# Kernel tuning notes

Hardware: AMD Instinct MI355X
Metric: run time of the kernel (lower is better)

The kernel has to match this reference:

```python
import jax, jax.numpy as jnp
import numpy as np
from jax import lax

V = 100000   # vocab
D = 300      # embedding / input_dim
H = 512      # hidden_dim per direction
T = 8192     # sequence length (batch_size hardcoded to 1 in the module)
TAG = 12     # len(tag_dict)
START = 10
STOP = 11
NEG = -10000.0


def setup_inputs() -> dict:
    key = jax.random.key(0)
    ks = jax.random.split(key, 11)
    s = 1.0 / np.sqrt(H)
    u = lambda k, shp: jax.random.uniform(k, shp, minval=-s, maxval=s)
    transition = jax.random.normal(ks[9], (TAG, TAG))
    transition = transition.at[:, START].set(NEG).at[STOP, :].set(NEG)
    return {
        "sent": jax.random.randint(ks[0], (T,), 0, V, dtype=jnp.int32),
        "emb": jax.random.normal(ks[1], (V, D)) * 0.1,
        "W_ih_f": u(ks[2], (4 * H, D)),
        "W_hh_f": u(ks[3], (4 * H, H)),
        "b_f": u(ks[4], (4 * H,)),
        "W_ih_b": u(ks[5], (4 * H, D)),
        "W_hh_b": u(ks[6], (4 * H, H)),
        "b_b": u(ks[7], (4 * H,)),
        "W_proj": u(ks[8], (TAG, 2 * H)),
        "b_proj": jnp.zeros((TAG,)),
        "transition": transition,
    }


def _lstm_dir(xs, Wih, Whh, b):
    # one-direction LSTM over [T, D] (batch=1 squeezed); torch gate order i,f,g,o
    def step(carry, x):
        h, c = carry
        g = x @ Wih.T + h @ Whh.T + b
        i, f, gg, o = jnp.split(g, 4)
        c = jax.nn.sigmoid(f) * c + jax.nn.sigmoid(i) * jnp.tanh(gg)
        h = jax.nn.sigmoid(o) * jnp.tanh(c)
        return (h, c), h
    z = jnp.zeros((H,), xs.dtype)
    _, hs = lax.scan(step, (z, z), xs)
    return hs


def reference(sent, emb, W_ih_f, W_hh_f, b_f, W_ih_b, W_hh_b, b_b, W_proj, b_proj, transition):
    x = emb[sent]  # [T, D]
    hf = _lstm_dir(x, W_ih_f, W_hh_f, b_f)                 # [T, H]
    hb = _lstm_dir(x[::-1], W_ih_b, W_hh_b, b_b)[::-1]     # [T, H]
    hh = jnp.concatenate([hf, hb], axis=-1)                # [T, 2H]
    feats = jax.nn.log_softmax(hh @ W_proj.T + b_proj, axis=-1)  # [T, TAG]

    # Viterbi decode (self.decode): max over previous tag + transition + emission
    def vstep(v, feat):
        tmp = v[:, None] + transition   # [TAG_prev, TAG_next]
        return tmp.max(axis=0) + feat, jnp.argmax(tmp, axis=0)
    v0 = jnp.full((TAG,), NEG).at[START].set(0.0)
    vT, ptrs = lax.scan(vstep, v0, feats)
    vT = vT + transition[:, STOP]
    score = vT.max()
    best = jnp.argmax(vT)

    # backtrace: best_tags[t] = ptrs[t][best_tags[t+1]], return best_tags[1:T] + [best]
    def back(tag, ptr):
        prev = ptr[tag]
        return prev, prev
    _, ys = lax.scan(back, best, ptrs, reverse=True)  # ys[t] = best_tags[t], t=0..T-1
    tags = jnp.concatenate([ys[1:], best[None]])
    return score, tags
```

## Files before the change

### kernel.cpp

```cpp
#include <hip/hip_runtime.h>
#include <stdint.h>

#define T_LEN 8192
#define HID 512
#define NTAG 12
#define START_TAG 10
#define STOP_TAG 11
#define NEGV -10000.0f

#define H_OFF     0u
#define FEATS_OFF 33554432u
#define CNT_OFF   33947648u

__device__ __forceinline__ float blo(uint32_t u) {
    union { uint32_t i; float f; } x; x.i = u << 16; return x.f;
}
__device__ __forceinline__ float bhi(uint32_t u) {
    union { uint32_t i; float f; } x; x.i = u & 0xffff0000u; return x.f;
}
__device__ __forceinline__ float b2f(uint16_t u) {
    union { uint32_t i; float f; } x; x.i = ((uint32_t)u) << 16; return x.f;
}
__device__ __forceinline__ uint32_t rne16(float f) {
    union { float f; uint32_t i; } x; x.f = f;
    uint32_t u = x.i + 0x7FFFu + ((x.i >> 16) & 1u);
    return u >> 16;
}
__device__ __forceinline__ uint32_t pk(float f0, float f1) {
    return rne16(f0) | (rne16(f1) << 16);
}
__device__ __forceinline__ float sigm(float x) { return 1.0f / (1.0f + expf(-x)); }

__global__ __launch_bounds__(256) void k_probe(
    const uint32_t* __restrict__ embw, const int* __restrict__ sent32, int* __restrict__ cnt)
{
    __shared__ int s_bf16, s_zero;
    const int tid = threadIdx.x;
    if (tid == 0) { s_bf16 = 0; s_zero = 0; }
    __syncthreads();
    uint32_t u = embw[tid * 97 + 5];
    float lo = b2f((uint16_t)(u & 0xFFFFu));
    float hi = b2f((uint16_t)(u >> 16));
    if (fabsf(lo) <= 8.0f && fabsf(hi) <= 8.0f) atomicAdd(&s_bf16, 1);
    if (sent32[2 * tid + 1] == 0) atomicAdd(&s_zero, 1);
    __syncthreads();
    if (tid == 0) {
        cnt[32] = (s_bf16 < 224) ? 1 : 0;
        cnt[33] = (s_zero >= 250) ? 1 : 0;
    }
    if (tid < 32) cnt[tid] = 0;
}

__global__ __launch_bounds__(512) void k_scan(
    const int* __restrict__ sent, const void* __restrict__ emb,
    const void* __restrict__ wih_f, const void* __restrict__ whh_f,
    const void* __restrict__ b_f,
    const void* __restrict__ wih_b, const void* __restrict__ whh_b,
    const void* __restrict__ b_b,
    float* __restrict__ harr, int* __restrict__ cnt)
{
    __shared__ uint16_t wlds[128 * 520];
    __shared__ float hbuf[512];
    __shared__ float partial[4][128];
    __shared__ float gbuf[128];
    __shared__ float xbuf[2][304];

    const int tid = threadIdx.x;
    const int dir = blockIdx.x >> 4;
    const int w   = blockIdx.x & 15;
    const int flagF32 = cnt[32];
    const int flag64  = cnt[33];
    const void* wih = dir ? wih_b : wih_f;
    const void* whh = dir ? whh_b : whh_f;
    const void* bb  = dir ? b_b  : b_f;
    float* hd = harr + (size_t)dir * T_LEN * HID;
    int* mycnt = cnt + dir * 16;

    const int rl = tid & 127;
    const int q  = tid >> 7;
    const int grow = w * 32 + (rl & 31) + 512 * (rl >> 5);

    if (flagF32) {
        const float4* src = (const float4*)((const float*)whh + (size_t)grow * HID + q * 128);
        uint4* dst = (uint4*)(&wlds[rl * 520 + q * 128]);
        #pragma unroll
        for (int kk = 0; kk < 16; ++kk) {
            float4 a = src[2 * kk], b = src[2 * kk + 1];
            uint4 o;
            o.x = pk(a.x, a.y); o.y = pk(a.z, a.w);
            o.z = pk(b.x, b.y); o.w = pk(b.z, b.w);
            dst[kk] = o;
        }
    } else {
        const uint4* src = (const uint4*)((const uint16_t*)whh + (size_t)grow * HID + q * 128);
        uint4* dst = (uint4*)(&wlds[rl * 520 + q * 128]);
        #pragma unroll
        for (int kk = 0; kk < 16; ++kk) dst[kk] = src[kk];
    }
    uint32_t wreg[38];
    if (flagF32) {
        const float* src = (const float*)wih + (size_t)grow * 300 + q * 76;
        #pragma unroll
        for (int kk = 0; kk < 38; ++kk) {
            int e = q * 76 + 2 * kk;
            float f0 = (e     < 300) ? src[2 * kk]     : 0.0f;
            float f1 = (e + 1 < 300) ? src[2 * kk + 1] : 0.0f;
            wreg[kk] = pk(f0, f1);
        }
    } else {
        const uint32_t* src = (const uint32_t*)((const uint16_t*)wih + (size_t)grow * 300 + q * 76);
        #pragma unroll
        for (int kk = 0; kk < 38; ++kk)
            wreg[kk] = (q * 76 + 2 * kk < 300) ? src[kk] : 0u;
    }
    const float bias = flagF32 ? ((const float*)bb)[grow] : b2f(((const uint16_t*)bb)[grow]);

    if (tid < 4) { xbuf[0][300 + tid] = 0.0f; xbuf[1][300 + tid] = 0.0f; }
    {
        int idx0 = dir ? (T_LEN - 1) : 0;
        if (tid < 150) {
            int tok = flag64 ? sent[2 * idx0] : sent[idx0];
            if (flagF32) {
                float2 v = ((const float2*)((const float*)emb + (size_t)tok * 300))[tid];
                xbuf[0][2 * tid] = v.x; xbuf[0][2 * tid + 1] = v.y;
            } else {
                uint32_t v = ((const uint32_t*)((const uint16_t*)emb + (size_t)tok * 300))[tid];
                xbuf[0][2 * tid] = blo(v); xbuf[0][2 * tid + 1] = bhi(v);
            }
        }
    }
    __syncthreads();

    float c = 0.0f;

    for (int ts = 0; ts < T_LEN; ++ts) {
        const int idx  = dir ? (T_LEN - 1 - ts) : ts;
        const int slot = ts & 1;

        uint32_t nxtu = 0; float2 nxtf = make_float2(0.0f, 0.0f);
        if (tid < 150) {
            int ts2  = (ts + 1 < T_LEN) ? (ts + 1) : 0;
            int idx2 = dir ? (T_LEN - 1 - ts2) : ts2;
            int tok2 = flag64 ? sent[2 * idx2] : sent[idx2];
            if (flagF32)
                nxtf = ((const float2*)((const float*)emb + (size_t)tok2 * 300))[tid];
            else
                nxtu = ((const uint32_t*)((const uint16_t*)emb + (size_t)tok2 * 300))[tid];
        }

        if (ts > 0) {
            if (tid == 0) {
                const int target = 16 * ts;
                while (__hip_atomic_load(mycnt, __ATOMIC_ACQUIRE, __HIP_MEMORY_SCOPE_AGENT) < target)
                    __builtin_amdgcn_s_sleep(2);
            }
            __syncthreads();
            const int pidx = dir ? (T_LEN - ts) : (ts - 1);
            hbuf[tid] = __hip_atomic_load(&hd[(size_t)pidx * HID + tid],
                                          __ATOMIC_RELAXED, __HIP_MEMORY_SCOPE_AGENT);
        } else {
            hbuf[tid] = 0.0f;
        }
        __syncthreads();

        {
            const uint4*  wrow = (const uint4*)(&wlds[rl * 520 + q * 128]);
            const float4* hseg = (const float4*)(&hbuf[q * 128]);
            float acc = 0.0f;
            #pragma unroll
            for (int kk = 0; kk < 16; ++kk) {
                uint4 wv = wrow[kk];
                float4 h0 = hseg[2 * kk];
                float4 h1 = hseg[2 * kk + 1];
                acc += blo(wv.x) * h0.x + bhi(wv.x) * h0.y;
                acc += blo(wv.y) * h0.z + bhi(wv.y) * h0.w;
                acc += blo(wv.z) * h1.x + bhi(wv.z) * h1.y;
                acc += blo(wv.w) * h1.z + bhi(wv.w) * h1.w;
            }
            const float2* xs2 = (const float2*)(&xbuf[slot][q * 76]);
            #pragma unroll
            for (int kk = 0; kk < 38; ++kk) {
                float2 xv = xs2[kk];
                acc += blo(wreg[kk]) * xv.x + bhi(wreg[kk]) * xv.y;
            }
            partial[q][rl] = acc;
        }
        __syncthreads();

        if (tid < 150) {
            if (flagF32) {
                xbuf[slot ^ 1][2 * tid] = nxtf.x; xbuf[slot ^ 1][2 * tid + 1] = nxtf.y;
            } else {
                xbuf[slot ^ 1][2 * tid] = blo(nxtu); xbuf[slot ^ 1][2 * tid + 1] = bhi(nxtu);
            }
        }
        if (tid < 128)
            gbuf[tid] = bias + partial[0][tid] + partial[1][tid]
                             + partial[2][tid] + partial[3][tid];
        __syncthreads();

        if (tid < 32) {
            float gi = gbuf[tid], gf = gbuf[32 + tid], gg = gbuf[64 + tid], go = gbuf[96 + tid];
            c = sigm(gf) * c + sigm(gi) * tanhf(gg);
            float h = sigm(go) * tanhf(c);
            __hip_atomic_store(&hd[(size_t)idx * HID + w * 32 + tid], h,
                               __ATOMIC_RELAXED, __HIP_MEMORY_SCOPE_AGENT);
        }
        __syncthreads();
        if (tid == 0)
            __hip_atomic_fetch_add(mycnt, 1, __ATOMIC_RELEASE, __HIP_MEMORY_SCOPE_AGENT);
    }
}

__global__ __launch_bounds__(256) void k_feats(
    const float* __restrict__ harr, const void* __restrict__ wproj,
    const void* __restrict__ bproj, const int* __restrict__ cnt,
    float* __restrict__ feats)
{
    const int flagF32 = cnt[32];
    const int lane = threadIdx.x & 63;
    const int t = blockIdx.x * 4 + (threadIdx.x >> 6);
    const float* hf = harr;
    const float* hb = harr + (size_t)T_LEN * HID;
    float z[NTAG];
    #pragma unroll
    for (int j = 0; j < NTAG; ++j) z[j] = 0.0f;
    if (flagF32) {
        const float* wp = (const float*)wproj;
        for (int kk = lane; kk < 2 * HID; kk += 64) {
            float hv = (kk < HID) ? hf[(size_t)t * HID + kk] : hb[(size_t)t * HID + kk - HID];
            #pragma unroll
            for (int j = 0; j < NTAG; ++j) z[j] += wp[j * 2 * HID + kk] * hv;
        }
    } else {
        const uint16_t* wp = (const uint16_t*)wproj;
        for (int kk = lane; kk < 2 * HID; kk += 64) {
            float hv = (kk < HID) ? hf[(size_t)t * HID + kk] : hb[(size_t)t * HID + kk - HID];
            #pragma unroll
            for (int j = 0; j < NTAG; ++j) z[j] += b2f(wp[j * 2 * HID + kk]) * hv;
        }
    }
    #pragma unroll
    for (int j = 0; j < NTAG; ++j) {
        #pragma unroll
        for (int s = 1; s < 64; s <<= 1) z[j] += __shfl_xor(z[j], s);
        z[j] += flagF32 ? ((const float*)bproj)[j] : b2f(((const uint16_t*)bproj)[j]);
    }
    float m = z[0];
    #pragma unroll
    for (int j = 1; j < NTAG; ++j) m = fmaxf(m, z[j]);
    float se = 0.0f;
    #pragma unroll
    for (int j = 0; j < NTAG; ++j) se += expf(z[j] - m);
    float lse = m + logf(se);
    if (lane == 0) {
        #pragma unroll
        for (int j = 0; j < NTAG; ++j)
            feats[(size_t)t * NTAG + j] = z[j] - lse;
    }
}

__global__ __launch_bounds__(64) void k_viterbi(
    const float* __restrict__ feats, const void* __restrict__ trans,
    const int* __restrict__ cnt, float* __restrict__ out)
{
    __shared__ unsigned long long prow[T_LEN];
    __shared__ float fbuf[448];
    const int flagF32 = cnt[32];
    const int l = threadIdx.x;
    const int jcol = (l < NTAG) ? l : 0;
    float trcol[NTAG], trstop[NTAG];
    if (flagF32) {
        const float* tr = (const float*)trans;
        #pragma unroll
        for (int i = 0; i < NTAG; ++i) { trcol[i] = tr[i * NTAG + jcol]; trstop[i] = tr[i * NTAG + STOP_TAG]; }
    } else {
        const uint16_t* tr = (const uint16_t*)trans;
        #pragma unroll
        for (int i = 0; i < NTAG; ++i) { trcol[i] = b2f(tr[i * NTAG + jcol]); trstop[i] = b2f(tr[i * NTAG + STOP_TAG]); }
    }
    float v[NTAG];
    #pragma unroll
    for (int i = 0; i < NTAG; ++i) v[i] = (i == START_TAG) ? 0.0f : NEGV;

    for (int t = 0; t < T_LEN; ++t) {
        if ((t & 31) == 0) {
            __syncthreads();
            #pragma unroll
            for (int r = 0; r < 6; ++r) {
                int g = l + r * 64;
                fbuf[g] = feats[t * NTAG + g];
            }
            __syncthreads();
        }
        float best = v[0] + trcol[0];
        int bi = 0;
        #pragma unroll
        for (int i = 1; i < NTAG; ++i) {
            float cand = v[i] + trcol[i];
            if (cand > best) { best = cand; bi = i; }
        }
        float newv = best + fbuf[(t & 31) * NTAG + jcol];
        unsigned long long contrib = (l < NTAG) ? ((unsigned long long)bi << (4 * l)) : 0ull;
        #pragma unroll
        for (int s = 1; s < 16; s <<= 1) contrib |= __shfl_xor(contrib, s);
        if (l == 0) prow[t] = contrib;
        #pragma unroll
        for (int i = 0; i < NTAG; ++i) v[i] = __shfl(newv, i);
    }

    if (l == 0) {
        float best = v[0] + trstop[0];
        int bt = 0;
        #pragma unroll
        for (int i = 1; i < NTAG; ++i) {
            float cand = v[i] + trstop[i];
            if (cand > best) { best = cand; bt = i; }
        }
        out[0] = best;
        int tag = bt;
        out[T_LEN] = (float)tag;
        unsigned long long row = prow[T_LEN - 1];
        for (int t = T_LEN - 1; t >= 1; --t) {
            unsigned long long nxt = (t > 1) ? prow[t - 1] : 0ull;
            tag = (int)((row >> (4 * tag)) & 15ull);
            out[t] = (float)tag;
            row = nxt;
        }
    }
}

extern "C" void kernel_launch(void* const* d_in, const int* in_sizes, int n_in,
                              void* d_out, int out_size, void* d_ws, size_t ws_size,
                              hipStream_t stream)
{
    const int*  sent  = (const int*)d_in[0];
    const void* emb   = d_in[1];
    const void* wih_f = d_in[2];
    const void* whh_f = d_in[3];
    const void* b_f   = d_in[4];
    const void* wih_b = d_in[5];
    const void* whh_b = d_in[6];
    const void* b_b   = d_in[7];
    const void* wproj = d_in[8];
    const void* bproj = d_in[9];
    const void* trans = d_in[10];

    char* ws = (char*)d_ws;
    float* harr  = (float*)(ws + H_OFF);
    float* feats = (float*)(ws + FEATS_OFF);
    int*   cnt   = (int*)(ws + CNT_OFF);
    float* out   = (float*)d_out;

    k_probe<<<1, 256, 0, stream>>>((const uint32_t*)emb, sent, cnt);
    k_scan<<<32, 512, 0, stream>>>(sent, emb, wih_f, whh_f, b_f,
                                   wih_b, whh_b, b_b, harr, cnt);
    k_feats<<<T_LEN / 4, 256, 0, stream>>>(harr, wproj, bproj, cnt, feats);
    k_viterbi<<<1, 64, 0, stream>>>(feats, trans, cnt, out);
}
```

Before: 33.95 ms.

## Replace counter barrier with per-element tagged h flags and register-resident weights

The recurrent scan now signals readiness per hidden element. Each h value is stored as a bf16 payload packed with the step index in the upper 16 bits, so consumers spin on the data word itself and the global counter with its acquire/release handshake goes away. W_hh moves from LDS into registers, the input projection is computed before the wait so it overlaps the spin, and the partial reduction drops one barrier by summing float4 partials in the gate threads. Gate nonlinearities use fast __expf forms. The risks are higher register pressure (launch bounds set to one block), h stored at bf16 precision, and the 16-bit step tag, which cannot exceed 65535 steps.

After: 40.36 ms. +18.9%, slower.

```diff
diff --git a/kernel.cpp b/kernel.cpp
--- a/kernel.cpp
+++ b/kernel.cpp
@@ -8,7 +8,7 @@
 #define STOP_TAG 11
 #define NEGV -10000.0f
 
-#define H_OFF     0u
+#define HX_OFF    0u
 #define FEATS_OFF 33554432u
 #define CNT_OFF   33947648u
 
@@ -29,7 +29,8 @@
 __device__ __forceinline__ uint32_t pk(float f0, float f1) {
     return rne16(f0) | (rne16(f1) << 16);
 }
-__device__ __forceinline__ float sigm(float x) { return 1.0f / (1.0f + expf(-x)); }
+__device__ __forceinline__ float fsig(float x) { return 1.0f / (1.0f + __expf(-x)); }
+__device__ __forceinline__ float ftanh(float x) { return 1.0f - 2.0f / (1.0f + __expf(2.0f * x)); }
 
 __global__ __launch_bounds__(256) void k_probe(
     const uint32_t* __restrict__ embw, const int* __restrict__ sent32, int* __restrict__ cnt)
@@ -51,19 +52,17 @@
     if (tid < 32) cnt[tid] = 0;
 }
 
-__global__ __launch_bounds__(512) void k_scan(
+__global__ __launch_bounds__(512, 1) void k_scan(
     const int* __restrict__ sent, const void* __restrict__ emb,
     const void* __restrict__ wih_f, const void* __restrict__ whh_f,
     const void* __restrict__ b_f,
     const void* __restrict__ wih_b, const void* __restrict__ whh_b,
     const void* __restrict__ b_b,
-    float* __restrict__ harr, int* __restrict__ cnt)
-{
-    __shared__ uint16_t wlds[128 * 520];
-    __shared__ float hbuf[512];
-    __shared__ float partial[4][128];
-    __shared__ float gbuf[128];
-    __shared__ float xbuf[2][304];
+    uint32_t* __restrict__ hx, int* __restrict__ cnt)
+{
+    __shared__ float  hbuf[512];
+    __shared__ float4 partial[128];
+    __shared__ float  xbuf[2][304];
 
     const int tid = threadIdx.x;
     const int dir = blockIdx.x >> 4;
@@ -73,31 +72,23 @@
     const void* wih = dir ? wih_b : wih_f;
     const void* whh = dir ? whh_b : whh_f;
     const void* bb  = dir ? b_b  : b_f;
-    float* hd = harr + (size_t)dir * T_LEN * HID;
-    int* mycnt = cnt + dir * 16;
+    uint32_t* hd = hx + (size_t)dir * T_LEN * HID;
 
     const int rl = tid & 127;
     const int q  = tid >> 7;
     const int grow = w * 32 + (rl & 31) + 512 * (rl >> 5);
 
+    uint32_t wh[64];
     if (flagF32) {
-        const float4* src = (const float4*)((const float*)whh + (size_t)grow * HID + q * 128);
-        uint4* dst = (uint4*)(&wlds[rl * 520 + q * 128]);
-        #pragma unroll
-        for (int kk = 0; kk < 16; ++kk) {
-            float4 a = src[2 * kk], b = src[2 * kk + 1];
-            uint4 o;
-            o.x = pk(a.x, a.y); o.y = pk(a.z, a.w);
-            o.z = pk(b.x, b.y); o.w = pk(b.z, b.w);
-            dst[kk] = o;
-        }
+        const float* src = (const float*)whh + (size_t)grow * HID + q * 128;
+        #pragma unroll
+        for (int kk = 0; kk < 64; ++kk) wh[kk] = pk(src[2 * kk], src[2 * kk + 1]);
     } else {
-        const uint4* src = (const uint4*)((const uint16_t*)whh + (size_t)grow * HID + q * 128);
-        uint4* dst = (uint4*)(&wlds[rl * 520 + q * 128]);
-        #pragma unroll
-        for (int kk = 0; kk < 16; ++kk) dst[kk] = src[kk];
-    }
-    uint32_t wreg[38];
+        const uint32_t* src = (const uint32_t*)((const uint16_t*)whh + (size_t)grow * HID + q * 128);
+        #pragma unroll
+        for (int kk = 0; kk < 64; ++kk) wh[kk] = src[kk];
+    }
+    uint32_t wi[38];
     if (flagF32) {
         const float* src = (const float*)wih + (size_t)grow * 300 + q * 76;
         #pragma unroll
@@ -105,13 +96,13 @@
             int e = q * 76 + 2 * kk;
             float f0 = (e     < 300) ? src[2 * kk]     : 0.0f;
             float f1 = (e + 1 < 300) ? src[2 * kk + 1] : 0.0f;
-            wreg[kk] = pk(f0, f1);
+            wi[kk] = pk(f0, f1);
         }
     } else {
         const uint32_t* src = (const uint32_t*)((const uint16_t*)wih + (size_t)grow * 300 + q * 76);
         #pragma unroll
         for (int kk = 0; kk < 38; ++kk)
-            wreg[kk] = (q * 76 + 2 * kk < 300) ? src[kk] : 0u;
+            wi[kk] = (q * 76 + 2 * kk < 300) ? src[kk] : 0u;
     }
     const float bias = flagF32 ? ((const float*)bb)[grow] : b2f(((const uint16_t*)bb)[grow]);
 
@@ -148,45 +139,42 @@
                 nxtu = ((const uint32_t*)((const uint16_t*)emb + (size_t)tok2 * 300))[tid];
         }
 
+        float xdot = (q == 0) ? bias : 0.0f;
+        {
+            const float2* xs2 = (const float2*)(&xbuf[slot][q * 76]);
+            #pragma unroll
+            for (int kk = 0; kk < 38; ++kk) {
+                float2 xv = xs2[kk];
+                xdot += blo(wi[kk]) * xv.x + bhi(wi[kk]) * xv.y;
+            }
+        }
+
         if (ts > 0) {
-            if (tid == 0) {
-                const int target = 16 * ts;
-                while (__hip_atomic_load(mycnt, __ATOMIC_ACQUIRE, __HIP_MEMORY_SCOPE_AGENT) < target)
-                    __builtin_amdgcn_s_sleep(2);
-            }
-            __syncthreads();
             const int pidx = dir ? (T_LEN - ts) : (ts - 1);
-            hbuf[tid] = __hip_atomic_load(&hd[(size_t)pidx * HID + tid],
-                                          __ATOMIC_RELAXED, __HIP_MEMORY_SCOPE_AGENT);
+            const uint32_t* src = hd + (size_t)pidx * HID + tid;
+            const uint32_t expect = (uint32_t)ts << 16;
+            uint32_t pv;
+            do {
+                pv = __hip_atomic_load(src, __ATOMIC_RELAXED, __HIP_MEMORY_SCOPE_AGENT);
+            } while ((pv & 0xFFFF0000u) != expect);
+            hbuf[tid] = blo(pv);
         } else {
             hbuf[tid] = 0.0f;
         }
         __syncthreads();
 
         {
-            const uint4*  wrow = (const uint4*)(&wlds[rl * 520 + q * 128]);
             const float4* hseg = (const float4*)(&hbuf[q * 128]);
-            float acc = 0.0f;
-            #pragma unroll
-            for (int kk = 0; kk < 16; ++kk) {
-                uint4 wv = wrow[kk];
-                float4 h0 = hseg[2 * kk];
-                float4 h1 = hseg[2 * kk + 1];
-                acc += blo(wv.x) * h0.x + bhi(wv.x) * h0.y;
-                acc += blo(wv.y) * h0.z + bhi(wv.y) * h0.w;
-                acc += blo(wv.z) * h1.x + bhi(wv.z) * h1.y;
-                acc += blo(wv.w) * h1.z + bhi(wv.w) * h1.w;
-            }
-            const float2* xs2 = (const float2*)(&xbuf[slot][q * 76]);
-            #pragma unroll
-            for (int kk = 0; kk < 38; ++kk) {
-                float2 xv = xs2[kk];
-                acc += blo(wreg[kk]) * xv.x + bhi(wreg[kk]) * xv.y;
-            }
-            partial[q][rl] = acc;
-        }
-        __syncthreads();
-
+            float acc = xdot;
+            #pragma unroll
+            for (int kk = 0; kk < 32; ++kk) {
+                float4 h4 = hseg[kk];
+                uint32_t a = wh[2 * kk], b = wh[2 * kk + 1];
+                acc += blo(a) * h4.x + bhi(a) * h4.y;
+                acc += blo(b) * h4.z + bhi(b) * h4.w;
+            }
+            ((float*)&partial[rl])[q] = acc;
+        }
         if (tid < 150) {
             if (flagF32) {
                 xbuf[slot ^ 1][2 * tid] = nxtf.x; xbuf[slot ^ 1][2 * tid + 1] = nxtf.y;
@@ -194,48 +182,50 @@
                 xbuf[slot ^ 1][2 * tid] = blo(nxtu); xbuf[slot ^ 1][2 * tid + 1] = bhi(nxtu);
             }
         }
-        if (tid < 128)
-            gbuf[tid] = bias + partial[0][tid] + partial[1][tid]
-                             + partial[2][tid] + partial[3][tid];
         __syncthreads();
 
         if (tid < 32) {
-            float gi = gbuf[tid], gf = gbuf[32 + tid], gg = gbuf[64 + tid], go = gbuf[96 + tid];
-            c = sigm(gf) * c + sigm(gi) * tanhf(gg);
-            float h = sigm(go) * tanhf(c);
-            __hip_atomic_store(&hd[(size_t)idx * HID + w * 32 + tid], h,
+            float4 pi = partial[tid],      pf = partial[32 + tid];
+            float4 pg = partial[64 + tid], po = partial[96 + tid];
+            float gi = pi.x + pi.y + pi.z + pi.w;
+            float gf = pf.x + pf.y + pf.z + pf.w;
+            float gg = pg.x + pg.y + pg.z + pg.w;
+            float go = po.x + po.y + po.z + po.w;
+            c = fsig(gf) * c + fsig(gi) * ftanh(gg);
+            float h = fsig(go) * ftanh(c);
+            uint32_t pkd = ((uint32_t)(ts + 1) << 16) | rne16(h);
+            __hip_atomic_store(&hd[(size_t)idx * HID + w * 32 + tid], pkd,
                                __ATOMIC_RELAXED, __HIP_MEMORY_SCOPE_AGENT);
         }
-        __syncthreads();
-        if (tid == 0)
-            __hip_atomic_fetch_add(mycnt, 1, __ATOMIC_RELEASE, __HIP_MEMORY_SCOPE_AGENT);
     }
 }
 
 __global__ __launch_bounds__(256) void k_feats(
-    const float* __restrict__ harr, const void* __restrict__ wproj,
+    const uint32_t* __restrict__ hx, const void* __restrict__ wproj,
     const void* __restrict__ bproj, const int* __restrict__ cnt,
     float* __restrict__ feats)
 {
     const int flagF32 = cnt[32];
     const int lane = threadIdx.x & 63;
     const int t = blockIdx.x * 4 + (threadIdx.x >> 6);
-    const float* hf = harr;
-    const float* hb = harr + (size_t)T_LEN * HID;
+    const uint32_t* hf = hx;
+    const uint32_t* hb = hx + (size_t)T_LEN * HID;
     float z[NTAG];
     #pragma unroll
     for (int j = 0; j < NTAG; ++j) z[j] = 0.0f;
     if (flagF32) {
         const float* wp = (const float*)wproj;
         for (int kk = lane; kk < 2 * HID; kk += 64) {
-            float hv = (kk < HID) ? hf[(size_t)t * HID + kk] : hb[(size_t)t * HID + kk - HID];
+            float hv = (kk < HID) ? blo(hf[(size_t)t * HID + kk])
+                                  : blo(hb[(size_t)t * HID + kk - HID]);
             #pragma unroll
             for (int j = 0; j < NTAG; ++j) z[j] += wp[j * 2 * HID + kk] * hv;
         }
     } else {
         const uint16_t* wp = (const uint16_t*)wproj;
         for (int kk = lane; kk < 2 * HID; kk += 64) {
-            float hv = (kk < HID) ? hf[(size_t)t * HID + kk] : hb[(size_t)t * HID + kk - HID];
+            float hv = (kk < HID) ? blo(hf[(size_t)t * HID + kk])
+                                  : blo(hb[(size_t)t * HID + kk - HID]);
             #pragma unroll
             for (int j = 0; j < NTAG; ++j) z[j] += b2f(wp[j * 2 * HID + kk]) * hv;
         }
@@ -347,14 +337,14 @@
     const void* trans = d_in[10];
 
     char* ws = (char*)d_ws;
-    float* harr  = (float*)(ws + H_OFF);
-    float* feats = (float*)(ws + FEATS_OFF);
-    int*   cnt   = (int*)(ws + CNT_OFF);
-    float* out   = (float*)d_out;
+    uint32_t* hx  = (uint32_t*)(ws + HX_OFF);
+    float* feats  = (float*)(ws + FEATS_OFF);
+    int*   cnt    = (int*)(ws + CNT_OFF);
+    float* out    = (float*)d_out;
 
     k_probe<<<1, 256, 0, stream>>>((const uint32_t*)emb, sent, cnt);
     k_scan<<<32, 512, 0, stream>>>(sent, emb, wih_f, whh_f, b_f,
-                                   wih_b, whh_b, b_b, harr, cnt);
-    k_feats<<<T_LEN / 4, 256, 0, stream>>>(harr, wproj, bproj, cnt, feats);
+                                   wih_b, whh_b, b_b, hx, cnt);
+    k_feats<<<T_LEN / 4, 256, 0, stream>>>(hx, wproj, bproj, cnt, feats);
     k_viterbi<<<1, 64, 0, stream>>>(feats, trans, cnt, out);
 }
```
